# Optimization experiments

Hardware: AMD Instinct MI355X
Metric: run time of the kernel (lower is better)

## Reference

```python
import jax, jax.numpy as jnp
import numpy as np


def setup_inputs() -> dict:
    key = jax.random.key(0)
    ks = jax.random.split(key, 6)
    N, D_IN, H, DH, N_ITEM = 4096, 512, 8, 128, 256
    x = jax.random.normal(ks[0], (N, D_IN), dtype=jnp.float32)
    y = jax.random.normal(ks[1], (N, D_IN), dtype=jnp.float32)
    # linear1/linear2 have NonNeg kernel constraint -> nonnegative weights
    W1 = jax.random.uniform(ks[2], (D_IN, H * DH), dtype=jnp.float32) * 0.05
    W2 = jax.random.uniform(ks[3], (D_IN, H * DH), dtype=jnp.float32) * 0.05
    W3 = jax.random.normal(ks[4], (D_IN, H * DH), dtype=jnp.float32) * 0.05
    # 1x1 conv with 1 output filter over the head axis == weighted sum over heads
    conv_w = jax.random.normal(ks[5], (H,), dtype=jnp.float32)
    return {"x": x, "y": y, "W1": W1, "W2": W2, "W3": W3,
            "conv_w": conv_w, "nItem": N_ITEM}


def reference(x, y, W1, W2, W3, conv_w, nItem):
    N = x.shape[0]
    H = conv_w.shape[0]
    Dh = W1.shape[1] // H
    nSet = N // nItem
    inv_sqrt = 1.0 / jnp.sqrt(jnp.asarray(Dh, dtype=x.dtype))

    q = (x @ W1).reshape(N, H, Dh).transpose(1, 0, 2)   # [H, N, Dh]
    k = (y @ W2).reshape(N, H, Dh).transpose(1, 0, 2)   # [H, N, Dh]
    v = (y @ W3).reshape(N, H, Dh).transpose(1, 0, 2)   # [H, N, Dh]

    # Full cross-set scores, as in the original: [H, N, N]
    scores = jnp.einsum('hnd,hmd->hnm', q, k) * inv_sqrt

    # Block-diagonal y2 matmul == per-set segmented matmul:
    # newx[h, n, s*Dh:(s+1)*Dh] = scores[h, n, s*nItem:(s+1)*nItem] @ v_set_s
    scores_s = scores.reshape(H, N, nSet, nItem)
    v_s = v.reshape(H, nSet, nItem, Dh)
    newx = jnp.einsum('hnsi,hsid->hnsd', scores_s, v_s) / nItem  # [H, N, nSet, Dh]

    # 1x1 conv mixing heads (single output filter, no bias)
    mixed = jnp.einsum('hnsd,h->nsd', newx, conv_w)  # [N, nSet, Dh]

    # isOnlySelf=False branch: reshape [N, nSet*Dh] -> [N, nSet, Dh]
    return mixed
```

## Files before the change

kernel.cpp:

```cpp
#include <hip/hip_runtime.h>
#include <stdint.h>
#include <stddef.h>


typedef short short8 __attribute__((ext_vector_type(8)));
typedef float f32x4 __attribute__((ext_vector_type(4)));

#define AS1 __attribute__((address_space(1)))
#define AS3 __attribute__((address_space(3)))

__device__ __forceinline__ void gl_lds16(const void* g, void* l) {
    __builtin_amdgcn_global_load_lds((AS1 void*)(uintptr_t)g, (AS3 void*)l, 16, 0, 0);
}

__device__ __forceinline__ short f2bf(float f) {
    union { float f; unsigned u; } v; v.f = f;
    unsigned r = v.u + 0x7FFFu + ((v.u >> 16) & 1u);
    return (short)(r >> 16);
}

__global__ __launch_bounds__(256)
void prep(const float* __restrict__ x, const float* __restrict__ y,
          const float* __restrict__ W1, const float* __restrict__ W2,
          const float* __restrict__ W3, short* __restrict__ xb,
          short* __restrict__ yb, short* __restrict__ w1t,
          short* __restrict__ w23t) {
    const int b = blockIdx.x, tid = threadIdx.x;
    if (b < 2048) {
        const float* in = (b < 1024) ? x : y;
        short* o = (b < 1024) ? xb : yb;
        const int i = (b & 1023) * 256 + tid;
        const float4* p = (const float4*)in + (size_t)i * 2;
        float4 a = p[0], c4 = p[1];
        short8 s8;
        s8[0] = f2bf(a.x);  s8[1] = f2bf(a.y);
        s8[2] = f2bf(a.z);  s8[3] = f2bf(a.w);
        s8[4] = f2bf(c4.x); s8[5] = f2bf(c4.y);
        s8[6] = f2bf(c4.z); s8[7] = f2bf(c4.w);
        *((short8*)o + i) = s8;
        return;
    }
    __shared__ float t[32][33];
    const float* W; short* Wt; int b3;
    if (b < 3072) {
        const int b2 = b - 2048;
        const int z = b2 >> 9;
        W = z ? W3 : W2;
        Wt = w23t + (size_t)z * 1024 * 512;
        b3 = b2 & 511;
    } else {
        W = W1; Wt = w1t; b3 = b - 3072;
    }
    const int bx = (b3 & 31) * 32, by = (b3 >> 5) * 32;
    const int tx = tid & 31, ty = tid >> 5;
    #pragma unroll
    for (int j = 0; j < 4; ++j)
        t[ty + j * 8][tx] = W[(size_t)(by + ty + j * 8) * 1024 + bx + tx];
    __syncthreads();
    #pragma unroll
    for (int j = 0; j < 4; ++j)
        Wt[(size_t)(bx + ty + j * 8) * 512 + by + tx] = f2bf(t[tx][ty + j * 8]);
}

template <int OUTMODE>
__device__ __forceinline__
void gemm_tile(const short* __restrict__ A, int lda,
               const short* __restrict__ Bt, int ldb,
               void* __restrict__ Cout, int ldc, int K,
               int bx, int by, float scale, char* smem) {
    short* sA = (short*)smem;
    short* sB = (short*)(smem + 8192);

    const int tid = threadIdx.x;
    const int wave = tid >> 6, lane = tid & 63;
    const int quad = lane >> 4, ml = lane & 15;
    const int m0 = by * 128, n0 = bx * 128;
    const int wm0 = (wave >> 1) * 64, wn0 = (wave & 1) * 64;
    const int srow = lane >> 2, skoff = (lane & 3) * 8;

    f32x4 acc[4][4];
    #pragma unroll
    for (int i = 0; i < 4; ++i)
        #pragma unroll
        for (int j = 0; j < 4; ++j) {
            acc[i][j][0] = 0.f; acc[i][j][1] = 0.f;
            acc[i][j][2] = 0.f; acc[i][j][3] = 0.f;
        }

    for (int kt = 0; kt < K; kt += 32) {
        #pragma unroll
        for (int ci = 0; ci < 4; ++ci) {
            const int c = wave + ci * 4;
            if (c < 8)
                gl_lds16(A + (size_t)(m0 + c * 16 + srow) * lda + kt + skoff,
                         (char*)sA + c * 1024 + lane * 16);
            else
                gl_lds16(Bt + (size_t)(n0 + (c - 8) * 16 + srow) * ldb + kt + skoff,
                         (char*)sB + (c - 8) * 1024 + lane * 16);
        }
        __syncthreads();

        short8 af[4], bfr[4];
        #pragma unroll
        for (int mt = 0; mt < 4; ++mt)
            af[mt] = *(const short8*)(sA + (wm0 + mt * 16 + ml) * 32 + quad * 8);
        #pragma unroll
        for (int nt = 0; nt < 4; ++nt)
            bfr[nt] = *(const short8*)(sB + (wn0 + nt * 16 + ml) * 32 + quad * 8);

        #pragma unroll
        for (int mt = 0; mt < 4; ++mt)
            #pragma unroll
            for (int nt = 0; nt < 4; ++nt)
                acc[mt][nt] = __builtin_amdgcn_mfma_f32_16x16x32_bf16(
                    af[mt], bfr[nt], acc[mt][nt], 0, 0, 0);
        __syncthreads();
    }

    #pragma unroll
    for (int mt = 0; mt < 4; ++mt)
        #pragma unroll
        for (int nt = 0; nt < 4; ++nt) {
            const int col = n0 + wn0 + nt * 16 + ml;
            #pragma unroll
            for (int r = 0; r < 4; ++r) {
                const int row = m0 + wm0 + mt * 16 + quad * 4 + r;
                float v = acc[mt][nt][r];
                if (OUTMODE == 2) v *= scale;
                if (OUTMODE == 0)
                    ((float*)Cout)[(size_t)row * ldc + col] = v;
                else
                    ((short*)Cout)[(size_t)row * ldc + col] = f2bf(v);
            }
        }
}

__global__ __launch_bounds__(256)
void stage_b(const short* __restrict__ yb, const short* __restrict__ w23t,
             const short* __restrict__ xb, const short* __restrict__ w1t,
             short* __restrict__ kvt, short* __restrict__ qb) {
    __shared__ char smem[16384];
    const int b = blockIdx.x;
    if (b < 512) {
        gemm_tile<1>(w23t, 512, yb, 512, kvt, 4096, 512,
                     b & 31, b >> 5, 1.f, smem);
    } else {
        const int b2 = b - 512;
        gemm_tile<1>(xb, 512, w1t, 512, qb, 1024, 512,
                     b2 & 7, b2 >> 3, 1.f, smem);
    }
}

__global__ __launch_bounds__(256)
void build_u(const short* __restrict__ kvt, const float* __restrict__ cw,
             short* __restrict__ Ut) {
    __shared__ char smem[16384];
    const int s = blockIdx.x, h = blockIdx.y;
    const float scale = cw[h] * (0.08838834764831845f / 256.0f);
    gemm_tile<2>(kvt + (size_t)(1024 + h * 128) * 4096 + s * 256, 4096,
                 kvt + (size_t)(h * 128) * 4096 + s * 256, 4096,
                 Ut + (size_t)(s * 128) * 1024 + h * 128, 1024, 256,
                 0, 0, scale, smem);
}

__global__ __launch_bounds__(256)
void gemm_out(const short* __restrict__ qb, const short* __restrict__ Ut,
              float* __restrict__ out) {
    __shared__ char smem[16384];
    gemm_tile<0>(qb, 1024, Ut, 1024, out, 2048, 1024,
                 blockIdx.x, blockIdx.y, 1.f, smem);
}

extern "C" void kernel_launch(void* const* d_in, const int* in_sizes, int n_in,
                              void* d_out, int out_size, void* d_ws, size_t ws_size,
                              hipStream_t stream) {
    const float* x  = (const float*)d_in[0];
    const float* y  = (const float*)d_in[1];
    const float* W1 = (const float*)d_in[2];
    const float* W2 = (const float*)d_in[3];
    const float* W3 = (const float*)d_in[4];
    const float* cw = (const float*)d_in[5];
    float* out = (float*)d_out;

    short* xb   = (short*)d_ws;
    short* yb   = xb   + (size_t)4096 * 512;
    short* w1t  = yb   + (size_t)4096 * 512;
    short* w23t = w1t  + (size_t)1024 * 512;
    short* kvt  = w23t + (size_t)2048 * 512;
    short* qb   = kvt  + (size_t)2048 * 4096;
    short* Ut   = qb   + (size_t)4096 * 1024;

    prep<<<3584, 256, 0, stream>>>(x, y, W1, W2, W3, xb, yb, w1t, w23t);
    stage_b<<<768, 256, 0, stream>>>(yb, w23t, xb, w1t, kvt, qb);
    build_u<<<dim3(16, 8), 256, 0, stream>>>(kvt, cw, Ut);
    gemm_out<<<dim3(16, 32), 256, 0, stream>>>(qb, Ut, out);
}
```

Before: 141.9 us.

## Reassociate output GEMM as x @ (W1 @ U) to drop the Q projection

Instead of computing Q = x@W1 and then Q@U, the code first folds W1 into the per-set head-mixed matrix U (a new build_m kernel computing M = U·W1 with K=1024), then computes out = x@M with K=512. This removes the separate Q projection GEMM and halves the reduction depth of the largest output GEMM. W1 no longer needs transposing, only bf16 conversion. It adds one serial kernel launch with a small grid of 64 blocks, and an extra bf16 rounding of the fused matrix M.

```diff
diff --git a/kernel.cpp b/kernel.cpp
--- a/kernel.cpp
+++ b/kernel.cpp
@@ -23,7 +23,7 @@
 void prep(const float* __restrict__ x, const float* __restrict__ y,
           const float* __restrict__ W1, const float* __restrict__ W2,
           const float* __restrict__ W3, short* __restrict__ xb,
-          short* __restrict__ yb, short* __restrict__ w1t,
+          short* __restrict__ yb, short* __restrict__ w1b,
           short* __restrict__ w23t) {
     const int b = blockIdx.x, tid = threadIdx.x;
     if (b < 2048) {
@@ -40,17 +40,24 @@
         *((short8*)o + i) = s8;
         return;
     }
+    if (b >= 3072) {
+        const int i = (b - 3072) * 256 + tid;
+        const float4* p = (const float4*)W1 + (size_t)i * 2;
+        float4 a = p[0], c4 = p[1];
+        short8 s8;
+        s8[0] = f2bf(a.x);  s8[1] = f2bf(a.y);
+        s8[2] = f2bf(a.z);  s8[3] = f2bf(a.w);
+        s8[4] = f2bf(c4.x); s8[5] = f2bf(c4.y);
+        s8[6] = f2bf(c4.z); s8[7] = f2bf(c4.w);
+        *((short8*)w1b + i) = s8;
+        return;
+    }
     __shared__ float t[32][33];
-    const float* W; short* Wt; int b3;
-    if (b < 3072) {
-        const int b2 = b - 2048;
-        const int z = b2 >> 9;
-        W = z ? W3 : W2;
-        Wt = w23t + (size_t)z * 1024 * 512;
-        b3 = b2 & 511;
-    } else {
-        W = W1; Wt = w1t; b3 = b - 3072;
-    }
+    const int b2 = b - 2048;
+    const int z = b2 >> 9;
+    const float* W = z ? W3 : W2;
+    short* Wt = w23t + (size_t)z * 1024 * 512;
+    const int b3 = b2 & 511;
     const int bx = (b3 & 31) * 32, by = (b3 >> 5) * 32;
     const int tx = tid & 31, ty = tid >> 5;
     #pragma unroll
@@ -136,19 +143,12 @@
 }
 
 __global__ __launch_bounds__(256)
-void stage_b(const short* __restrict__ yb, const short* __restrict__ w23t,
-             const short* __restrict__ xb, const short* __restrict__ w1t,
-             short* __restrict__ kvt, short* __restrict__ qb) {
+void stage_kv(const short* __restrict__ yb, const short* __restrict__ w23t,
+              short* __restrict__ kvt) {
     __shared__ char smem[16384];
     const int b = blockIdx.x;
-    if (b < 512) {
-        gemm_tile<1>(w23t, 512, yb, 512, kvt, 4096, 512,
-                     b & 31, b >> 5, 1.f, smem);
-    } else {
-        const int b2 = b - 512;
-        gemm_tile<1>(xb, 512, w1t, 512, qb, 1024, 512,
-                     b2 & 7, b2 >> 3, 1.f, smem);
-    }
+    gemm_tile<1>(w23t, 512, yb, 512, kvt, 4096, 512,
+                 b & 31, b >> 5, 1.f, smem);
 }
 
 __global__ __launch_bounds__(256)
@@ -164,10 +164,18 @@
 }
 
 __global__ __launch_bounds__(256)
-void gemm_out(const short* __restrict__ qb, const short* __restrict__ Ut,
+void build_m(const short* __restrict__ Ut, const short* __restrict__ w1b,
+             short* __restrict__ M) {
+    __shared__ char smem[16384];
+    gemm_tile<1>(Ut, 1024, w1b, 1024, M, 512, 1024,
+                 blockIdx.x, blockIdx.y, 1.f, smem);
+}
+
+__global__ __launch_bounds__(256)
+void gemm_out(const short* __restrict__ xb, const short* __restrict__ M,
               float* __restrict__ out) {
     __shared__ char smem[16384];
-    gemm_tile<0>(qb, 1024, Ut, 1024, out, 2048, 1024,
+    gemm_tile<0>(xb, 512, M, 512, out, 2048, 512,
                  blockIdx.x, blockIdx.y, 1.f, smem);
 }
 
@@ -184,14 +192,15 @@
 
     short* xb   = (short*)d_ws;
     short* yb   = xb   + (size_t)4096 * 512;
-    short* w1t  = yb   + (size_t)4096 * 512;
-    short* w23t = w1t  + (size_t)1024 * 512;
-    short* kvt  = w23t + (size_t)2048 * 512;
-    short* qb   = kvt  + (size_t)2048 * 4096;
-    short* Ut   = qb   + (size_t)4096 * 1024;
-
-    prep<<<3584, 256, 0, stream>>>(x, y, W1, W2, W3, xb, yb, w1t, w23t);
-    stage_b<<<768, 256, 0, stream>>>(yb, w23t, xb, w1t, kvt, qb);
+    short* w23t = yb   + (size_t)4096 * 512;
+    short* w1b  = w23t + (size_t)2048 * 512;
+    short* kvt  = w1b  + (size_t)512 * 1024;
+    short* Ut   = kvt  + (size_t)2048 * 4096;
+    short* M    = Ut   + (size_t)2048 * 1024;
+
+    prep<<<3328, 256, 0, stream>>>(x, y, W1, W2, W3, xb, yb, w1b, w23t);
+    stage_kv<<<512, 256, 0, stream>>>(yb, w23t, kvt);
     build_u<<<dim3(16, 8), 256, 0, stream>>>(kvt, cw, Ut);
-    gemm_out<<<dim3(16, 32), 256, 0, stream>>>(qb, Ut, out);
-}
+    build_m<<<dim3(4, 16), 256, 0, stream>>>(Ut, w1b, M);
+    gemm_out<<<dim3(16, 32), 256, 0, stream>>>(xb, M, out);
+}
```

New measurement: 147.5 us. +4.0%, slower.
